# Kernel optimization log

Hardware: AMD Instinct MI355X
Metric: run time of the kernel (lower is better)

## Reference

```python
import jax, jax.numpy as jnp
import numpy as np

N0 = 1373      # hardcoded node-type split in the original forward
TAO = 0.4
EPS = 1e-12


def _l2norm(x, axis):
    # matches torch F.normalize(p=2): x / max(||x||, eps)
    n = jnp.sqrt(jnp.sum(x * x, axis=axis, keepdims=True))
    return x / jnp.maximum(n, EPS)


def setup_inputs() -> dict:
    key = jax.random.key(0)
    ks = jax.random.split(key, 12)
    N, E, D_IN, F, H, D = 20000, 320000, 256, 32, 8, 32
    feat = jax.random.normal(ks[0], (N, D_IN), jnp.float32)
    sloc = jax.random.normal(ks[1], (N, D), jnp.float32)
    topo_fea = jax.random.normal(ks[2], (N, D), jnp.float32)
    src = jax.random.randint(ks[3], (E,), 0, N)
    dst = jax.random.randint(ks[4], (E,), 0, N)
    e_feat = jax.random.randint(ks[5], (E,), 0, 4)
    s = 1.0 / np.sqrt(D_IN)
    W_proj0 = jax.random.normal(ks[6], (D_IN, H * F), jnp.float32) * s
    W_proj1 = jax.random.normal(ks[7], (D_IN, H * F), jnp.float32) * s
    W_prob = jax.random.normal(ks[8], (H, F, F), jnp.float32) * (1.0 / np.sqrt(F))
    W_res0 = jax.random.normal(ks[9], (D_IN, H * F), jnp.float32) * s
    W_res1 = jax.random.normal(ks[10], (D_IN, H * F), jnp.float32) * s
    etype_attn = jnp.ones((4,), jnp.float32)
    return dict(feat=feat, sloc=sloc, topo_fea=topo_fea, src=src, dst=dst,
                e_feat=e_feat, W_proj0=W_proj0, W_proj1=W_proj1, W_prob=W_prob,
                W_res0=W_res0, W_res1=W_res1, etype_attn=etype_attn)


def reference(feat, sloc, topo_fea, src, dst, e_feat,
              W_proj0, W_proj1, W_prob, W_res0, W_res1, etype_attn):
    N = feat.shape[0]
    H, F = W_prob.shape[0], W_prob.shape[2]
    sloc3 = sloc[:, None, :]        # (N,1,D) -- .unsqueeze(1)
    topo3 = topo_fea[:, None, :]

    # per-type node projection
    feat_src = jnp.concatenate(
        [feat[:N0] @ W_proj0, feat[N0:] @ W_proj1], axis=0).reshape(N, H, F)
    # per-head attention feature: softmax(tanh(fc4prob_i(.)), dim=feat)
    ft_attn = jax.nn.softmax(
        jnp.tanh(jnp.einsum('nhf,hfg->nhg', feat_src, W_prob)), axis=2)
    # F.normalize over the NODE dimension (dim=0), as in original
    ft_norm = _l2norm(feat_src, axis=0)

    sloc_n = _l2norm(sloc3, axis=2)
    topo_n = _l2norm(topo3, axis=2)

    # edge attention scores
    a = jnp.sum(ft_attn[dst] * ft_norm[src], axis=2, keepdims=True)   # (E,H,1)
    cos_s = jnp.sum(sloc_n[src] * sloc_n[dst], axis=2, keepdims=True)  # (E,1,1)
    cos_t = jnp.sum(topo_n[src] * topo_n[dst], axis=2, keepdims=True)
    sim = (TAO * cos_s + (1.0 - TAO) * cos_t + 1.0) / 2.0             # (E,1,1)
    e = (sim * a * etype_attn[e_feat][:, None, None])[:, :, 0]        # (E,H)

    # edge softmax: segment softmax over incoming edges of each dst node
    m = jax.ops.segment_max(e, dst, num_segments=N)                   # (N,H)
    ex = jnp.exp(e - m[dst])
    z = jax.ops.segment_sum(ex, dst, num_segments=N)
    att = ex / z[dst]                                                 # (E,H)

    # three u_mul_e + sum aggregations
    aw = att[:, :, None]                                              # (E,H,1)
    rst = jax.ops.segment_sum(feat_src[src] * aw, dst, num_segments=N)  # (N,H,F)
    sl2 = jax.ops.segment_sum(sloc3[src] * aw, dst, num_segments=N)     # (N,H,D)
    tp2 = jax.ops.segment_sum(topo3[src] * aw, dst, num_segments=N)     # (N,H,D)

    resval = jnp.concatenate(
        [feat[:N0] @ W_res0, feat[N0:] @ W_res1], axis=0).reshape(N, H, F)
    out_fea = jax.nn.relu(rst + resval).mean(axis=1)   # (N,F)
    out_sloc = (sl2 + sloc3).mean(axis=1)              # (N,D)
    out_topo = (tp2 + topo3).mean(axis=1)              # (N,D)
    return out_fea, out_sloc, out_topo
```

## Files before the change

### kernel.cpp

```cpp
#include <hip/hip_runtime.h>
#include <math.h>

#define HN0 1373
#define BM 128
#define BN 128
#define BK 32
#define LDT 40

typedef __attribute__((ext_vector_type(8))) short short8;
typedef __attribute__((ext_vector_type(4))) float f32x4;

__device__ inline unsigned short f2bf(float f) {
  unsigned int u = __float_as_uint(f);
  unsigned int r = (u + 0x7FFFu + ((u >> 16) & 1u)) >> 16;
  return (unsigned short)r;
}
__device__ inline float bflo(unsigned int u) { return __uint_as_float(u << 16); }
__device__ inline float bfhi(unsigned int u) { return __uint_as_float(u & 0xFFFF0000u); }

__device__ inline uint4 pack8bf(float4 a, float4 b) {
  uint4 o;
  o.x = (unsigned)f2bf(a.x) | ((unsigned)f2bf(a.y) << 16);
  o.y = (unsigned)f2bf(a.z) | ((unsigned)f2bf(a.w) << 16);
  o.z = (unsigned)f2bf(b.x) | ((unsigned)f2bf(b.y) << 16);
  o.w = (unsigned)f2bf(b.z) | ((unsigned)f2bf(b.w) << 16);
  return o;
}

__global__ __launch_bounds__(256) void prep(
    const float* __restrict__ Wp0, const float* __restrict__ Wr0,
    const float* __restrict__ Wp1, const float* __restrict__ Wr1,
    unsigned short* __restrict__ BTw,
    const float* __restrict__ sloc, const float* __restrict__ topo,
    unsigned short* __restrict__ slt, unsigned short* __restrict__ sltn,
    const int* __restrict__ dst, int* __restrict__ deg, int N, int E) {
  __shared__ float T[64][72];
  int b = blockIdx.x;
  int tid = threadIdx.x;
  int nodeBlocks = (N + 7) / 8;
  if (b < 64) {
    int mat = b >> 4;
    int t16 = b & 15;
    int kT = (t16 & 3) * 64;
    int nT = (t16 >> 2) * 64;
    const float* W = (mat == 0) ? Wp0 : (mat == 1) ? Wr0 : (mat == 2) ? Wp1 : Wr1;
    int g = mat >> 1;
    int nbase = (mat & 1) * 256;
    int r = tid >> 2;
    int cb = (tid & 3) * 16;
    const float* srcp = W + (size_t)(kT + r) * 256 + nT + cb;
#pragma unroll
    for (int q = 0; q < 4; ++q) {
      float4 v = *reinterpret_cast<const float4*>(srcp + q * 4);
      T[cb + q * 4 + 0][r] = v.x;
      T[cb + q * 4 + 1][r] = v.y;
      T[cb + q * 4 + 2][r] = v.z;
      T[cb + q * 4 + 3][r] = v.w;
    }
    __syncthreads();
    int nl = tid >> 2;
    int kb = (tid & 3) * 16;
    unsigned int pk[8];
#pragma unroll
    for (int q = 0; q < 8; ++q) {
      unsigned short lo = f2bf(T[nl][kb + q * 2]);
      unsigned short hi = f2bf(T[nl][kb + q * 2 + 1]);
      pk[q] = (unsigned)lo | ((unsigned)hi << 16);
    }
    unsigned short* dstp = BTw + (size_t)g * 512 * 256 + (size_t)(nbase + nT + nl) * 256 + kT + kb;
    *reinterpret_cast<uint4*>(dstp) = make_uint4(pk[0], pk[1], pk[2], pk[3]);
    *reinterpret_cast<uint4*>(dstp + 8) = make_uint4(pk[4], pk[5], pk[6], pk[7]);
  } else if (b < 64 + nodeBlocks) {
    int node = (b - 64) * 8 + (tid >> 5);
    int d = tid & 31;
    if (node >= N) return;
    float s = sloc[(size_t)node * 32 + d];
    float t = topo[(size_t)node * 32 + d];
    float ss = s * s, tt = t * t;
#pragma unroll
    for (int m = 16; m >= 1; m >>= 1) {
      ss += __shfl_xor(ss, m);
      tt += __shfl_xor(tt, m);
    }
    float is = 1.f / fmaxf(sqrtf(ss), 1e-12f);
    float it = 1.f / fmaxf(sqrtf(tt), 1e-12f);
    slt[(size_t)node * 64 + d] = f2bf(s);
    slt[(size_t)node * 64 + 32 + d] = f2bf(t);
    sltn[(size_t)node * 64 + d] = f2bf(s * is);
    sltn[(size_t)node * 64 + 32 + d] = f2bf(t * it);
  } else {
    int e = (b - 64 - nodeBlocks) * 256 + tid;
    if (e < E) atomicAdd(&deg[dst[e]], 1);
  }
}

__global__ __launch_bounds__(256) void gemm_scan(
    const float* __restrict__ A, const unsigned short* __restrict__ BTw,
    unsigned short* __restrict__ feat_bf, unsigned short* __restrict__ resval,
    const int* __restrict__ deg, int* __restrict__ start, int* __restrict__ bsum,
    int G, int N) {
  int b = blockIdx.x;
  int tid = threadIdx.x;
  if (b >= G) {
    __shared__ int buf[256];
    int b2 = b - G;
    int gid = b2 * 256 + tid;
    int v = (gid < N) ? deg[gid] : 0;
    buf[tid] = v;
    __syncthreads();
    for (int off = 1; off < 256; off <<= 1) {
      int t = (tid >= off) ? buf[tid - off] : 0;
      __syncthreads();
      buf[tid] += t;
      __syncthreads();
    }
    if (gid < N) start[gid] = buf[tid] - v;
    if (tid == 255) bsum[b2] = buf[255];
    return;
  }
  __shared__ __align__(16) unsigned short As[BM * LDT];
  __shared__ __align__(16) unsigned short Bs[BN * LDT];
  int lane = tid & 63;
  int w = tid >> 6;
  int wr = w >> 1, wc = w & 1;

  int g0t = (HN0 + BM - 1) / BM;
  int bx = b >> 2;
  int colBase = (b & 3) * BN;
  bool g1 = bx >= g0t;
  int rowBase = g1 ? HN0 + (bx - g0t) * BM : bx * BM;
  int rowEnd = g1 ? N : HN0;
  const unsigned short* BT = BTw + (g1 ? (size_t)512 * 256 : 0);

  int r0 = tid >> 2;
  int kp = (tid & 3) << 3;
  int ar1 = min(rowBase + r0, rowEnd - 1);
  int ar2 = min(rowBase + r0 + 64, rowEnd - 1);
  const float* aP1 = A + (size_t)ar1 * 256 + kp;
  const float* aP2 = A + (size_t)ar2 * 256 + kp;
  const unsigned short* bP1 = BT + (size_t)(colBase + r0) * 256 + kp;
  const unsigned short* bP2 = bP1 + (size_t)64 * 256;
  int wo1 = r0 * LDT + kp;
  int wo2 = (r0 + 64) * LDT + kp;

  int q = lane >> 4;
  int fr = lane & 15;
  int aOff = (wr * 64 + fr) * LDT + q * 8;
  int bOff = (wc * 64 + fr) * LDT + q * 8;

  f32x4 acc[4][4] = {};

  float4 fa1a = *reinterpret_cast<const float4*>(aP1);
  float4 fa1b = *reinterpret_cast<const float4*>(aP1 + 4);
  float4 fa2a = *reinterpret_cast<const float4*>(aP2);
  float4 fa2b = *reinterpret_cast<const float4*>(aP2 + 4);
  uint4 rb1 = *reinterpret_cast<const uint4*>(bP1);
  uint4 rb2 = *reinterpret_cast<const uint4*>(bP2);

  for (int t = 0; t < 8; ++t) {
    *reinterpret_cast<uint4*>(&As[wo1]) = pack8bf(fa1a, fa1b);
    *reinterpret_cast<uint4*>(&As[wo2]) = pack8bf(fa2a, fa2b);
    *reinterpret_cast<uint4*>(&Bs[wo1]) = rb1;
    *reinterpret_cast<uint4*>(&Bs[wo2]) = rb2;
    __syncthreads();
    if (t < 7) {
      int ko = (t + 1) * BK;
      fa1a = *reinterpret_cast<const float4*>(aP1 + ko);
      fa1b = *reinterpret_cast<const float4*>(aP1 + ko + 4);
      fa2a = *reinterpret_cast<const float4*>(aP2 + ko);
      fa2b = *reinterpret_cast<const float4*>(aP2 + ko + 4);
      rb1 = *reinterpret_cast<const uint4*>(bP1 + ko);
      rb2 = *reinterpret_cast<const uint4*>(bP2 + ko);
    }
    short8 af[4], bf4[4];
#pragma unroll
    for (int i = 0; i < 4; ++i) {
      af[i] = *reinterpret_cast<const short8*>(&As[aOff + i * 16 * LDT]);
      bf4[i] = *reinterpret_cast<const short8*>(&Bs[bOff + i * 16 * LDT]);
    }
#pragma unroll
    for (int i = 0; i < 4; ++i)
#pragma unroll
      for (int j = 0; j < 4; ++j)
        acc[i][j] = __builtin_amdgcn_mfma_f32_16x16x32_bf16(af[i], bf4[j], acc[i][j], 0, 0, 0);
    __syncthreads();
  }

  unsigned short* outp = (colBase < 256) ? feat_bf : resval;
  int cOff = colBase & 255;
#pragma unroll
  for (int i = 0; i < 4; ++i) {
    int rb = rowBase + wr * 64 + i * 16 + q * 4;
#pragma unroll
    for (int j = 0; j < 4; ++j) {
      int col = cOff + wc * 64 + j * 16 + fr;
      f32x4 v = acc[i][j];
#pragma unroll
      for (int rr = 0; rr < 4; ++rr) {
        int r = rb + rr;
        if (r < rowEnd) outp[(size_t)r * 256 + col] = f2bf(v[rr]);
      }
    }
  }
}

__global__ __launch_bounds__(256) void attn_mid(
    const unsigned short* __restrict__ feat_bf, const float* __restrict__ W_prob,
    unsigned short* __restrict__ ft_attn, float* __restrict__ col_ss,
    int* __restrict__ bsum, int nb, int nAttn, int N) {
  int tid = threadIdx.x;
  if ((int)blockIdx.x >= nAttn) {
    __shared__ int buf[128];
    if (tid < nb) buf[tid] = bsum[tid];
    __syncthreads();
    if (tid == 0) {
      int run = 0;
      for (int i = 0; i < nb; ++i) { int v = buf[i]; buf[i] = run; run += v; }
    }
    __syncthreads();
    if (tid < nb) bsum[tid] = buf[tid];
    return;
  }
  __shared__ float fsL[16 * 256];
  int h = tid >> 5, g = tid & 31;
  float wreg[32];
#pragma unroll
  for (int f = 0; f < 32; ++f) wreg[f] = W_prob[h * 1024 + f * 32 + g];
  int nodeBase = blockIdx.x * 16;
  float ssp = 0.f;
  for (int i = 0; i < 16; ++i) {
    int n = nodeBase + i;
    float v = (n < N) ? __uint_as_float((unsigned)feat_bf[(size_t)n * 256 + tid] << 16) : 0.f;
    fsL[i * 256 + tid] = v;
    ssp += v * v;
  }
  atomicAdd(&col_ss[tid], ssp);
  __syncthreads();
  for (int i = 0; i < 16; ++i) {
    int n = nodeBase + i;
    if (n >= N) break;
    const float* fr = &fsL[i * 256 + h * 32];
    float t0 = 0.f, t1 = 0.f, t2 = 0.f, t3 = 0.f;
#pragma unroll
    for (int f = 0; f < 8; ++f) {
      t0 = fmaf(fr[f * 4 + 0], wreg[f * 4 + 0], t0);
      t1 = fmaf(fr[f * 4 + 1], wreg[f * 4 + 1], t1);
      t2 = fmaf(fr[f * 4 + 2], wreg[f * 4 + 2], t2);
      t3 = fmaf(fr[f * 4 + 3], wreg[f * 4 + 3], t3);
    }
    float t = (t0 + t1) + (t2 + t3);
    float e2 = __expf(2.f * t);
    t = 1.f - 2.f * __builtin_amdgcn_rcpf(e2 + 1.f);
    float ex = __expf(t);
    float sm = ex;
#pragma unroll
    for (int s = 16; s >= 1; s >>= 1) sm += __shfl_xor(sm, s);
    ft_attn[(size_t)n * 256 + tid] = f2bf(ex * __builtin_amdgcn_rcpf(sm));
  }
}

__global__ __launch_bounds__(256) void fill_sim(
    const int* __restrict__ src, const int* __restrict__ dst,
    const int* __restrict__ e_feat, const float* __restrict__ etype_attn,
    const unsigned short* __restrict__ sltn,
    const int* __restrict__ start, const int* __restrict__ bsum,
    int* __restrict__ cursor, int2* __restrict__ csr, int E) {
  int tid = threadIdx.x;
  int j = tid & 3;
  int e = blockIdx.x * 64 + (tid >> 2);
  if (e >= E) return;
  int s = src[e], d = dst[e];
  const unsigned short* ps = sltn + (size_t)s * 64 + j * 16;
  const unsigned short* pd = sltn + (size_t)d * 64 + j * 16;
  uint4 a0 = *reinterpret_cast<const uint4*>(ps);
  uint4 a1 = *reinterpret_cast<const uint4*>(ps + 8);
  uint4 b0 = *reinterpret_cast<const uint4*>(pd);
  uint4 b1 = *reinterpret_cast<const uint4*>(pd + 8);
  float u = bflo(a0.x) * bflo(b0.x) + bfhi(a0.x) * bfhi(b0.x) +
            bflo(a0.y) * bflo(b0.y) + bfhi(a0.y) * bfhi(b0.y) +
            bflo(a0.z) * bflo(b0.z) + bfhi(a0.z) * bfhi(b0.z) +
            bflo(a0.w) * bflo(b0.w) + bfhi(a0.w) * bfhi(b0.w) +
            bflo(a1.x) * bflo(b1.x) + bfhi(a1.x) * bfhi(b1.x) +
            bflo(a1.y) * bflo(b1.y) + bfhi(a1.y) * bfhi(b1.y) +
            bflo(a1.z) * bflo(b1.z) + bfhi(a1.z) * bfhi(b1.z) +
            bflo(a1.w) * bflo(b1.w) + bfhi(a1.w) * bfhi(b1.w);
  u *= (j < 2) ? 0.4f : 0.6f;
  u += __shfl_xor(u, 1);
  u += __shfl_xor(u, 2);
  if (j == 0) {
    float sim = fmaf(u, 0.5f, 0.5f);
    float wv = sim * etype_attn[e_feat[e]];
    int pos = start[d] + bsum[d >> 8] + atomicAdd(&cursor[d], 1);
    csr[pos] = make_int2(s, __float_as_int(wv));
  }
}

#define LOADIDX(K, V, W)                                                       \
  do {                                                                         \
    int2 c_ = csr[s0 + (K)];                                                   \
    V = c_.x;                                                                  \
    W = __int_as_float(c_.y);                                                  \
  } while (0)

#define GATHER(V, FP, SL, TP)                                                  \
  do {                                                                         \
    FP = *reinterpret_cast<const uint2*>(feat_bf + (size_t)(V) * 256 + fb);    \
    const unsigned short* sp_ = slt + (size_t)(V) * 64 + db;                   \
    SL = *reinterpret_cast<const uint2*>(sp_);                                 \
    TP = *reinterpret_cast<const uint2*>(sp_ + 32);                            \
  } while (0)

#define CONSUME(W, FP, SL, TP)                                                 \
  do {                                                                         \
    float fs0 = bflo(FP.x), fs1 = bfhi(FP.x);                                  \
    float fs2 = bflo(FP.y), fs3 = bfhi(FP.y);                                  \
    float pa = ai4.x * fs0 + ai4.y * fs1 + ai4.z * fs2 + ai4.w * fs3;          \
    pa += __shfl_xor(pa, 1);                                                   \
    pa += __shfl_xor(pa, 2);                                                   \
    pa += __shfl_xor(pa, 4);                                                   \
    float p = __expf(pa * (W));                                                \
    l += p;                                                                    \
    accf.x = fmaf(p, fs0, accf.x); accf.y = fmaf(p, fs1, accf.y);              \
    accf.z = fmaf(p, fs2, accf.z); accf.w = fmaf(p, fs3, accf.w);              \
    accs.x = fmaf(p, bflo(SL.x), accs.x); accs.y = fmaf(p, bfhi(SL.x), accs.y);\
    accs.z = fmaf(p, bflo(SL.y), accs.z); accs.w = fmaf(p, bfhi(SL.y), accs.w);\
    acct.x = fmaf(p, bflo(TP.x), acct.x); acct.y = fmaf(p, bfhi(TP.x), acct.y);\
    acct.z = fmaf(p, bflo(TP.y), acct.z); acct.w = fmaf(p, bfhi(TP.y), acct.w);\
  } while (0)

__global__ __launch_bounds__(128) void edge_aggregate(
    const unsigned short* __restrict__ feat_bf, const unsigned short* __restrict__ resval,
    const unsigned short* __restrict__ ft_attn, const float* __restrict__ col_ss,
    const unsigned short* __restrict__ slt,
    const float* __restrict__ sloc, const float* __restrict__ topo,
    const int* __restrict__ start, const int* __restrict__ bsum,
    const int* __restrict__ deg, const int2* __restrict__ csr,
    float* __restrict__ out, int N) {
  int wave = threadIdx.x >> 6;
  int n = blockIdx.x * 2 + wave;
  if (n >= N) return;
  int lane = threadIdx.x & 63;
  int j = lane & 7;
  int fb = (lane >> 3) * 32 + j * 4;
  int db = j * 4;

  uint2 at2 = *reinterpret_cast<const uint2*>(ft_attn + (size_t)n * 256 + fb);
  float4 cs4 = *reinterpret_cast<const float4*>(col_ss + fb);
  float4 icn4 = make_float4(1.f / fmaxf(sqrtf(cs4.x), 1e-12f),
                            1.f / fmaxf(sqrtf(cs4.y), 1e-12f),
                            1.f / fmaxf(sqrtf(cs4.z), 1e-12f),
                            1.f / fmaxf(sqrtf(cs4.w), 1e-12f));
  float4 ai4 = make_float4(bflo(at2.x) * icn4.x, bfhi(at2.x) * icn4.y,
                           bflo(at2.y) * icn4.z, bfhi(at2.y) * icn4.w);
  float l = 0.f;
  float4 accf = make_float4(0.f, 0.f, 0.f, 0.f);
  float4 accs = make_float4(0.f, 0.f, 0.f, 0.f);
  float4 acct = make_float4(0.f, 0.f, 0.f, 0.f);
  int s0 = start[n] + bsum[n >> 8];
  int dg = deg[n];

  int vA = 0, vB = 0, vC = 0;
  float wA = 0.f, wB = 0.f, wC = 0.f;
  uint2 fpA = make_uint2(0u, 0u), fpB = make_uint2(0u, 0u), fpC = make_uint2(0u, 0u);
  uint2 slA = make_uint2(0u, 0u), slB = make_uint2(0u, 0u), slC = make_uint2(0u, 0u);
  uint2 tpA = make_uint2(0u, 0u), tpB = make_uint2(0u, 0u), tpC = make_uint2(0u, 0u);
  if (dg > 0) { LOADIDX(0, vA, wA); GATHER(vA, fpA, slA, tpA); }
  if (dg > 1) { LOADIDX(1, vB, wB); GATHER(vB, fpB, slB, tpB); }
  if (dg > 2) { LOADIDX(2, vC, wC); GATHER(vC, fpC, slC, tpC); }
  int i = 0;
  for (; i + 2 < dg; i += 3) {
    CONSUME(wA, fpA, slA, tpA);
    if (i + 3 < dg) { LOADIDX(i + 3, vA, wA); GATHER(vA, fpA, slA, tpA); }
    CONSUME(wB, fpB, slB, tpB);
    if (i + 4 < dg) { LOADIDX(i + 4, vB, wB); GATHER(vB, fpB, slB, tpB); }
    CONSUME(wC, fpC, slC, tpC);
    if (i + 5 < dg) { LOADIDX(i + 5, vC, wC); GATHER(vC, fpC, slC, tpC); }
  }
  if (i < dg) CONSUME(wA, fpA, slA, tpA);
  if (i + 1 < dg) CONSUME(wB, fpB, slB, tpB);

  float invl = (l > 0.f) ? 1.f / l : 0.f;

  uint2 res2 = *reinterpret_cast<const uint2*>(resval + (size_t)n * 256 + fb);
  float4 of = make_float4(fmaxf(fmaf(accf.x, invl, bflo(res2.x)), 0.f),
                          fmaxf(fmaf(accf.y, invl, bfhi(res2.x)), 0.f),
                          fmaxf(fmaf(accf.z, invl, bflo(res2.y)), 0.f),
                          fmaxf(fmaf(accf.w, invl, bfhi(res2.y)), 0.f));
  float4 os = make_float4(accs.x * invl, accs.y * invl, accs.z * invl, accs.w * invl);
  float4 ot = make_float4(acct.x * invl, acct.y * invl, acct.z * invl, acct.w * invl);
#pragma unroll
  for (int msk = 8; msk <= 32; msk <<= 1) {
    of.x += __shfl_xor(of.x, msk); of.y += __shfl_xor(of.y, msk);
    of.z += __shfl_xor(of.z, msk); of.w += __shfl_xor(of.w, msk);
    os.x += __shfl_xor(os.x, msk); os.y += __shfl_xor(os.y, msk);
    os.z += __shfl_xor(os.z, msk); os.w += __shfl_xor(os.w, msk);
    ot.x += __shfl_xor(ot.x, msk); ot.y += __shfl_xor(ot.y, msk);
    ot.z += __shfl_xor(ot.z, msk); ot.w += __shfl_xor(ot.w, msk);
  }
  if (lane < 8) {
    float4 sln = *reinterpret_cast<const float4*>(sloc + (size_t)n * 32 + db);
    float4 tpn = *reinterpret_cast<const float4*>(topo + (size_t)n * 32 + db);
    float4 o0 = make_float4(of.x * 0.125f, of.y * 0.125f, of.z * 0.125f, of.w * 0.125f);
    float4 o1 = make_float4(fmaf(os.x, 0.125f, sln.x), fmaf(os.y, 0.125f, sln.y),
                            fmaf(os.z, 0.125f, sln.z), fmaf(os.w, 0.125f, sln.w));
    float4 o2 = make_float4(fmaf(ot.x, 0.125f, tpn.x), fmaf(ot.y, 0.125f, tpn.y),
                            fmaf(ot.z, 0.125f, tpn.z), fmaf(ot.w, 0.125f, tpn.w));
    *reinterpret_cast<float4*>(out + (size_t)n * 32 + db) = o0;
    *reinterpret_cast<float4*>(out + (size_t)N * 32 + (size_t)n * 32 + db) = o1;
    *reinterpret_cast<float4*>(out + (size_t)2 * N * 32 + (size_t)n * 32 + db) = o2;
  }
}

extern "C" void kernel_launch(void* const* d_in, const int* in_sizes, int n_in,
                              void* d_out, int out_size, void* d_ws, size_t ws_size,
                              hipStream_t stream) {
  const float* feat = (const float*)d_in[0];
  const float* sloc = (const float*)d_in[1];
  const float* topo = (const float*)d_in[2];
  const int* src = (const int*)d_in[3];
  const int* dst = (const int*)d_in[4];
  const int* e_feat = (const int*)d_in[5];
  const float* W_proj0 = (const float*)d_in[6];
  const float* W_proj1 = (const float*)d_in[7];
  const float* W_prob = (const float*)d_in[8];
  const float* W_res0 = (const float*)d_in[9];
  const float* W_res1 = (const float*)d_in[10];
  const float* etype_attn = (const float*)d_in[11];
  int E = in_sizes[3];
  int N = in_sizes[1] / 32;
  float* out = (float*)d_out;

  char* ws = (char*)d_ws;
  size_t off = 0;
  auto alloc = [&](size_t bytes) -> char* {
    char* p = ws + off;
    off += (bytes + 255) & ~(size_t)255;
    return p;
  };
  int* deg = (int*)alloc((size_t)N * 4);
  int* cursor = (int*)alloc((size_t)N * 4);
  float* col_ss = (float*)alloc(256 * 4);
  size_t zeroBytes = ((char*)col_ss + 256 * 4) - (char*)deg;
  int* startArr = (int*)alloc(((size_t)N + 1) * 4);
  int* bsum = (int*)alloc(128 * 4);
  int2* csr = (int2*)alloc((size_t)E * 8);
  unsigned short* feat_bf = (unsigned short*)alloc((size_t)N * 256 * 2);
  unsigned short* slt = (unsigned short*)alloc((size_t)N * 64 * 2);
  unsigned short* sltn = (unsigned short*)alloc((size_t)N * 64 * 2);
  unsigned short* resval = (unsigned short*)alloc((size_t)N * 256 * 2);
  unsigned short* ft_attn = (unsigned short*)alloc((size_t)N * 256 * 2);
  unsigned short* BTw = (unsigned short*)alloc((size_t)2 * 512 * 256 * 2);

  hipMemsetAsync(deg, 0, zeroBytes, stream);

  int nodeBlocks = (N + 7) / 8;
  int degBlocks = (E + 255) / 256;
  prep<<<64 + nodeBlocks + degBlocks, 256, 0, stream>>>(
      W_proj0, W_res0, W_proj1, W_res1, BTw, sloc, topo, slt, sltn, dst, deg, N, E);

  int g0t = (HN0 + BM - 1) / BM;
  int g1t = (N - HN0 + BM - 1) / BM;
  int G = (g0t + g1t) * 4;
  int nb = (N + 255) / 256;
  gemm_scan<<<G + nb, 256, 0, stream>>>(feat, BTw, feat_bf, resval,
                                        deg, startArr, bsum, G, N);

  int nAttn = (N + 15) / 16;
  attn_mid<<<nAttn + 1, 256, 0, stream>>>(feat_bf, W_prob, ft_attn, col_ss,
                                          bsum, nb, nAttn, N);

  fill_sim<<<(E + 63) / 64, 256, 0, stream>>>(src, dst, e_feat, etype_attn, sltn,
                                              startArr, bsum, cursor, csr, E);

  edge_aggregate<<<(N + 1) / 2, 128, 0, stream>>>(feat_bf, resval, ft_attn, col_ss,
                                                  slt, sloc, topo, startArr, bsum,
                                                  deg, csr, out, N);
}
```

Before: 175.3 us.

## Fuse gather rows, merge fill into attn kernel, atomic block-scan offsets, deeper prefetch

Projected features and raw sloc/topo are stored together in one interleaved row (stride 320), so each neighbor gather in edge aggregation reads a single row instead of two separate arrays. The block-sum scan becomes an atomic counter in the scan blocks. Because neighbor order in the CSR is arbitrary anyway, block offsets no longer need to be sorted, which removes the separate serial scan step. The edge-fill work is merged into the attention kernel launch, saving one launch. The GEMM grid is reordered into groups of eight row tiles per column tile for L2 reuse of the B tiles. The edge-aggregation prefetch depth goes from three to four. The risks are a padded grid with idle early-exit blocks and higher register pressure in the aggregate loop.

```diff
diff --git a/kernel.cpp b/kernel.cpp
--- a/kernel.cpp
+++ b/kernel.cpp
@@ -6,6 +6,7 @@
 #define BN 128
 #define BK 32
 #define LDT 40
+#define FSTR 320
 
 typedef __attribute__((ext_vector_type(8))) short short8;
 typedef __attribute__((ext_vector_type(4))) float f32x4;
@@ -32,7 +33,7 @@
     const float* __restrict__ Wp1, const float* __restrict__ Wr1,
     unsigned short* __restrict__ BTw,
     const float* __restrict__ sloc, const float* __restrict__ topo,
-    unsigned short* __restrict__ slt, unsigned short* __restrict__ sltn,
+    unsigned short* __restrict__ fused, unsigned short* __restrict__ sltn,
     const int* __restrict__ dst, int* __restrict__ deg, int N, int E) {
   __shared__ float T[64][72];
   int b = blockIdx.x;
@@ -84,8 +85,8 @@
     }
     float is = 1.f / fmaxf(sqrtf(ss), 1e-12f);
     float it = 1.f / fmaxf(sqrtf(tt), 1e-12f);
-    slt[(size_t)node * 64 + d] = f2bf(s);
-    slt[(size_t)node * 64 + 32 + d] = f2bf(t);
+    fused[(size_t)node * FSTR + 256 + d] = f2bf(s);
+    fused[(size_t)node * FSTR + 288 + d] = f2bf(t);
     sltn[(size_t)node * 64 + d] = f2bf(s * is);
     sltn[(size_t)node * 64 + 32 + d] = f2bf(t * it);
   } else {
@@ -96,14 +97,14 @@
 
 __global__ __launch_bounds__(256) void gemm_scan(
     const float* __restrict__ A, const unsigned short* __restrict__ BTw,
-    unsigned short* __restrict__ feat_bf, unsigned short* __restrict__ resval,
+    unsigned short* __restrict__ fused, unsigned short* __restrict__ resval,
     const int* __restrict__ deg, int* __restrict__ start, int* __restrict__ bsum,
-    int G, int N) {
+    int* __restrict__ gctr, int Gpad, int R, int N) {
   int b = blockIdx.x;
   int tid = threadIdx.x;
-  if (b >= G) {
+  if (b >= Gpad) {
     __shared__ int buf[256];
-    int b2 = b - G;
+    int b2 = b - Gpad;
     int gid = b2 * 256 + tid;
     int v = (gid < N) ? deg[gid] : 0;
     buf[tid] = v;
@@ -115,9 +116,15 @@
       __syncthreads();
     }
     if (gid < N) start[gid] = buf[tid] - v;
-    if (tid == 255) bsum[b2] = buf[255];
+    if (tid == 255) bsum[b2] = atomicAdd(gctr, buf[255]);
     return;
   }
+  int r8 = b & 7;
+  int c = (b >> 3) & 3;
+  int bx = (b >> 5) * 8 + r8;
+  if (bx >= R) return;
+  int colBase = c * BN;
+
   __shared__ __align__(16) unsigned short As[BM * LDT];
   __shared__ __align__(16) unsigned short Bs[BN * LDT];
   int lane = tid & 63;
@@ -125,8 +132,6 @@
   int wr = w >> 1, wc = w & 1;
 
   int g0t = (HN0 + BM - 1) / BM;
-  int bx = b >> 2;
-  int colBase = (b & 3) * BN;
   bool g1 = bx >= g0t;
   int rowBase = g1 ? HN0 + (bx - g0t) * BM : bx * BM;
   int rowEnd = g1 ? N : HN0;
@@ -186,7 +191,7 @@
     __syncthreads();
   }
 
-  unsigned short* outp = (colBase < 256) ? feat_bf : resval;
+  bool isFeat = (colBase < 256);
   int cOff = colBase & 255;
 #pragma unroll
   for (int i = 0; i < 4; ++i) {
@@ -198,27 +203,53 @@
 #pragma unroll
       for (int rr = 0; rr < 4; ++rr) {
         int r = rb + rr;
-        if (r < rowEnd) outp[(size_t)r * 256 + col] = f2bf(v[rr]);
+        if (r < rowEnd) {
+          if (isFeat) fused[(size_t)r * FSTR + col] = f2bf(v[rr]);
+          else        resval[(size_t)r * 256 + col] = f2bf(v[rr]);
+        }
       }
     }
   }
 }
 
-__global__ __launch_bounds__(256) void attn_mid(
-    const unsigned short* __restrict__ feat_bf, const float* __restrict__ W_prob,
+__global__ __launch_bounds__(256) void attn_fill(
+    const unsigned short* __restrict__ fused, const float* __restrict__ W_prob,
     unsigned short* __restrict__ ft_attn, float* __restrict__ col_ss,
-    int* __restrict__ bsum, int nb, int nAttn, int N) {
+    const int* __restrict__ src, const int* __restrict__ dst,
+    const int* __restrict__ e_feat, const float* __restrict__ etype_attn,
+    const unsigned short* __restrict__ sltn,
+    const int* __restrict__ start, const int* __restrict__ bsum,
+    int* __restrict__ cursor, int2* __restrict__ csr,
+    int nAttn, int N, int E) {
   int tid = threadIdx.x;
   if ((int)blockIdx.x >= nAttn) {
-    __shared__ int buf[128];
-    if (tid < nb) buf[tid] = bsum[tid];
-    __syncthreads();
-    if (tid == 0) {
-      int run = 0;
-      for (int i = 0; i < nb; ++i) { int v = buf[i]; buf[i] = run; run += v; }
-    }
-    __syncthreads();
-    if (tid < nb) bsum[tid] = buf[tid];
+    int j = tid & 3;
+    int e = ((int)blockIdx.x - nAttn) * 64 + (tid >> 2);
+    if (e >= E) return;
+    int s = src[e], d = dst[e];
+    const unsigned short* ps = sltn + (size_t)s * 64 + j * 16;
+    const unsigned short* pd = sltn + (size_t)d * 64 + j * 16;
+    uint4 a0 = *reinterpret_cast<const uint4*>(ps);
+    uint4 a1 = *reinterpret_cast<const uint4*>(ps + 8);
+    uint4 b0 = *reinterpret_cast<const uint4*>(pd);
+    uint4 b1 = *reinterpret_cast<const uint4*>(pd + 8);
+    float u = bflo(a0.x) * bflo(b0.x) + bfhi(a0.x) * bfhi(b0.x) +
+              bflo(a0.y) * bflo(b0.y) + bfhi(a0.y) * bfhi(b0.y) +
+              bflo(a0.z) * bflo(b0.z) + bfhi(a0.z) * bfhi(b0.z) +
+              bflo(a0.w) * bflo(b0.w) + bfhi(a0.w) * bfhi(b0.w) +
+              bflo(a1.x) * bflo(b1.x) + bfhi(a1.x) * bfhi(b1.x) +
+              bflo(a1.y) * bflo(b1.y) + bfhi(a1.y) * bfhi(b1.y) +
+              bflo(a1.z) * bflo(b1.z) + bfhi(a1.z) * bfhi(b1.z) +
+              bflo(a1.w) * bflo(b1.w) + bfhi(a1.w) * bfhi(b1.w);
+    u *= (j < 2) ? 0.4f : 0.6f;
+    u += __shfl_xor(u, 1);
+    u += __shfl_xor(u, 2);
+    if (j == 0) {
+      float sim = fmaf(u, 0.5f, 0.5f);
+      float wv = sim * etype_attn[e_feat[e]];
+      int pos = start[d] + bsum[d >> 8] + atomicAdd(&cursor[d], 1);
+      csr[pos] = make_int2(s, __float_as_int(wv));
+    }
     return;
   }
   __shared__ float fsL[16 * 256];
@@ -230,7 +261,7 @@
   float ssp = 0.f;
   for (int i = 0; i < 16; ++i) {
     int n = nodeBase + i;
-    float v = (n < N) ? __uint_as_float((unsigned)feat_bf[(size_t)n * 256 + tid] << 16) : 0.f;
+    float v = (n < N) ? __uint_as_float((unsigned)fused[(size_t)n * FSTR + tid] << 16) : 0.f;
     fsL[i * 256 + tid] = v;
     ssp += v * v;
   }
@@ -259,42 +290,6 @@
   }
 }
 
-__global__ __launch_bounds__(256) void fill_sim(
-    const int* __restrict__ src, const int* __restrict__ dst,
-    const int* __restrict__ e_feat, const float* __restrict__ etype_attn,
-    const unsigned short* __restrict__ sltn,
-    const int* __restrict__ start, const int* __restrict__ bsum,
-    int* __restrict__ cursor, int2* __restrict__ csr, int E) {
-  int tid = threadIdx.x;
-  int j = tid & 3;
-  int e = blockIdx.x * 64 + (tid >> 2);
-  if (e >= E) return;
-  int s = src[e], d = dst[e];
-  const unsigned short* ps = sltn + (size_t)s * 64 + j * 16;
-  const unsigned short* pd = sltn + (size_t)d * 64 + j * 16;
-  uint4 a0 = *reinterpret_cast<const uint4*>(ps);
-  uint4 a1 = *reinterpret_cast<const uint4*>(ps + 8);
-  uint4 b0 = *reinterpret_cast<const uint4*>(pd);
-  uint4 b1 = *reinterpret_cast<const uint4*>(pd + 8);
-  float u = bflo(a0.x) * bflo(b0.x) + bfhi(a0.x) * bfhi(b0.x) +
-            bflo(a0.y) * bflo(b0.y) + bfhi(a0.y) * bfhi(b0.y) +
-            bflo(a0.z) * bflo(b0.z) + bfhi(a0.z) * bfhi(b0.z) +
-            bflo(a0.w) * bflo(b0.w) + bfhi(a0.w) * bfhi(b0.w) +
-            bflo(a1.x) * bflo(b1.x) + bfhi(a1.x) * bfhi(b1.x) +
-            bflo(a1.y) * bflo(b1.y) + bfhi(a1.y) * bfhi(b1.y) +
-            bflo(a1.z) * bflo(b1.z) + bfhi(a1.z) * bfhi(b1.z) +
-            bflo(a1.w) * bflo(b1.w) + bfhi(a1.w) * bfhi(b1.w);
-  u *= (j < 2) ? 0.4f : 0.6f;
-  u += __shfl_xor(u, 1);
-  u += __shfl_xor(u, 2);
-  if (j == 0) {
-    float sim = fmaf(u, 0.5f, 0.5f);
-    float wv = sim * etype_attn[e_feat[e]];
-    int pos = start[d] + bsum[d >> 8] + atomicAdd(&cursor[d], 1);
-    csr[pos] = make_int2(s, __float_as_int(wv));
-  }
-}
-
 #define LOADIDX(K, V, W)                                                       \
   do {                                                                         \
     int2 c_ = csr[s0 + (K)];                                                   \
@@ -304,10 +299,10 @@
 
 #define GATHER(V, FP, SL, TP)                                                  \
   do {                                                                         \
-    FP = *reinterpret_cast<const uint2*>(feat_bf + (size_t)(V) * 256 + fb);    \
-    const unsigned short* sp_ = slt + (size_t)(V) * 64 + db;                   \
-    SL = *reinterpret_cast<const uint2*>(sp_);                                 \
-    TP = *reinterpret_cast<const uint2*>(sp_ + 32);                            \
+    const unsigned short* r_ = fused + (size_t)(V) * FSTR;                     \
+    FP = *reinterpret_cast<const uint2*>(r_ + fb);                             \
+    SL = *reinterpret_cast<const uint2*>(r_ + 256 + db);                       \
+    TP = *reinterpret_cast<const uint2*>(r_ + 288 + db);                       \
   } while (0)
 
 #define CONSUME(W, FP, SL, TP)                                                 \
@@ -329,9 +324,8 @@
   } while (0)
 
 __global__ __launch_bounds__(128) void edge_aggregate(
-    const unsigned short* __restrict__ feat_bf, const unsigned short* __restrict__ resval,
+    const unsigned short* __restrict__ fused, const unsigned short* __restrict__ resval,
     const unsigned short* __restrict__ ft_attn, const float* __restrict__ col_ss,
-    const unsigned short* __restrict__ slt,
     const float* __restrict__ sloc, const float* __restrict__ topo,
     const int* __restrict__ start, const int* __restrict__ bsum,
     const int* __restrict__ deg, const int2* __restrict__ csr,
@@ -359,25 +353,30 @@
   int s0 = start[n] + bsum[n >> 8];
   int dg = deg[n];
 
-  int vA = 0, vB = 0, vC = 0;
-  float wA = 0.f, wB = 0.f, wC = 0.f;
-  uint2 fpA = make_uint2(0u, 0u), fpB = make_uint2(0u, 0u), fpC = make_uint2(0u, 0u);
-  uint2 slA = make_uint2(0u, 0u), slB = make_uint2(0u, 0u), slC = make_uint2(0u, 0u);
-  uint2 tpA = make_uint2(0u, 0u), tpB = make_uint2(0u, 0u), tpC = make_uint2(0u, 0u);
+  int vA = 0, vB = 0, vC = 0, vD = 0;
+  float wA = 0.f, wB = 0.f, wC = 0.f, wD = 0.f;
+  uint2 fpA, fpB, fpC, fpD, slA, slB, slC, slD, tpA, tpB, tpC, tpD;
+  fpA = fpB = fpC = fpD = make_uint2(0u, 0u);
+  slA = slB = slC = slD = make_uint2(0u, 0u);
+  tpA = tpB = tpC = tpD = make_uint2(0u, 0u);
   if (dg > 0) { LOADIDX(0, vA, wA); GATHER(vA, fpA, slA, tpA); }
   if (dg > 1) { LOADIDX(1, vB, wB); GATHER(vB, fpB, slB, tpB); }
   if (dg > 2) { LOADIDX(2, vC, wC); GATHER(vC, fpC, slC, tpC); }
+  if (dg > 3) { LOADIDX(3, vD, wD); GATHER(vD, fpD, slD, tpD); }
   int i = 0;
-  for (; i + 2 < dg; i += 3) {
+  for (; i + 3 < dg; i += 4) {
     CONSUME(wA, fpA, slA, tpA);
-    if (i + 3 < dg) { LOADIDX(i + 3, vA, wA); GATHER(vA, fpA, slA, tpA); }
+    if (i + 4 < dg) { LOADIDX(i + 4, vA, wA); GATHER(vA, fpA, slA, tpA); }
     CONSUME(wB, fpB, slB, tpB);
-    if (i + 4 < dg) { LOADIDX(i + 4, vB, wB); GATHER(vB, fpB, slB, tpB); }
+    if (i + 5 < dg) { LOADIDX(i + 5, vB, wB); GATHER(vB, fpB, slB, tpB); }
     CONSUME(wC, fpC, slC, tpC);
-    if (i + 5 < dg) { LOADIDX(i + 5, vC, wC); GATHER(vC, fpC, slC, tpC); }
+    if (i + 6 < dg) { LOADIDX(i + 6, vC, wC); GATHER(vC, fpC, slC, tpC); }
+    CONSUME(wD, fpD, slD, tpD);
+    if (i + 7 < dg) { LOADIDX(i + 7, vD, wD); GATHER(vD, fpD, slD, tpD); }
   }
   if (i < dg) CONSUME(wA, fpA, slA, tpA);
   if (i + 1 < dg) CONSUME(wB, fpB, slB, tpB);
+  if (i + 2 < dg) CONSUME(wC, fpC, slC, tpC);
 
   float invl = (l > 0.f) ? 1.f / l : 0.f;
 
@@ -440,12 +439,12 @@
   int* deg = (int*)alloc((size_t)N * 4);
   int* cursor = (int*)alloc((size_t)N * 4);
   float* col_ss = (float*)alloc(256 * 4);
-  size_t zeroBytes = ((char*)col_ss + 256 * 4) - (char*)deg;
+  int* gctr = (int*)alloc(256);
+  size_t zeroBytes = ((char*)gctr + 256) - (char*)deg;
   int* startArr = (int*)alloc(((size_t)N + 1) * 4);
   int* bsum = (int*)alloc(128 * 4);
   int2* csr = (int2*)alloc((size_t)E * 8);
-  unsigned short* feat_bf = (unsigned short*)alloc((size_t)N * 256 * 2);
-  unsigned short* slt = (unsigned short*)alloc((size_t)N * 64 * 2);
+  unsigned short* fused = (unsigned short*)alloc((size_t)N * FSTR * 2);
   unsigned short* sltn = (unsigned short*)alloc((size_t)N * 64 * 2);
   unsigned short* resval = (unsigned short*)alloc((size_t)N * 256 * 2);
   unsigned short* ft_attn = (unsigned short*)alloc((size_t)N * 256 * 2);
@@ -456,23 +455,23 @@
   int nodeBlocks = (N + 7) / 8;
   int degBlocks = (E + 255) / 256;
   prep<<<64 + nodeBlocks + degBlocks, 256, 0, stream>>>(
-      W_proj0, W_res0, W_proj1, W_res1, BTw, sloc, topo, slt, sltn, dst, deg, N, E);
+      W_proj0, W_res0, W_proj1, W_res1, BTw, sloc, topo, fused, sltn, dst, deg, N, E);
 
   int g0t = (HN0 + BM - 1) / BM;
   int g1t = (N - HN0 + BM - 1) / BM;
-  int G = (g0t + g1t) * 4;
+  int R = g0t + g1t;
+  int Gpad = ((R + 7) / 8) * 32;
   int nb = (N + 255) / 256;
-  gemm_scan<<<G + nb, 256, 0, stream>>>(feat, BTw, feat_bf, resval,
-                                        deg, startArr, bsum, G, N);
+  gemm_scan<<<Gpad + nb, 256, 0, stream>>>(feat, BTw, fused, resval,
+                                           deg, startArr, bsum, gctr, Gpad, R, N);
 
   int nAttn = (N + 15) / 16;
-  attn_mid<<<nAttn + 1, 256, 0, stream>>>(feat_bf, W_prob, ft_attn, col_ss,
-                                          bsum, nb, nAttn, N);
-
-  fill_sim<<<(E + 63) / 64, 256, 0, stream>>>(src, dst, e_feat, etype_attn, sltn,
-                                              startArr, bsum, cursor, csr, E);
-
-  edge_aggregate<<<(N + 1) / 2, 128, 0, stream>>>(feat_bf, resval, ft_attn, col_ss,
-                                                  slt, sloc, topo, startArr, bsum,
+  int fillBlocks = (E + 63) / 64;
+  attn_fill<<<nAttn + fillBlocks, 256, 0, stream>>>(
+      fused, W_prob, ft_attn, col_ss, src, dst, e_feat, etype_attn, sltn,
+      startArr, bsum, cursor, csr, nAttn, N, E);
+
+  edge_aggregate<<<(N + 1) / 2, 128, 0, stream>>>(fused, resval, ft_attn, col_ss,
+                                                  sloc, topo, startArr, bsum,
                                                   deg, csr, out, N);
 }
```

Result: faster. 169.9 us (-3.1%).

## Replace serial block-sum scan with atomic offsets and merge attention with CSR fill

Applied to the files above, without the earlier changes.

Each scan block in gemm_scan now claims its base offset in the CSR with an atomicAdd on a zeroed global counter, instead of a later single-block serial prefix over block sums. With that dependency gone, the attention-feature kernel and the edge-similarity/CSR-fill kernel are merged into one launch, removing one kernel launch and its serialization. The GEMM blocks are also remapped so groups of 8 row tiles share column tiles, for better L2 reuse of the B operand, with padding blocks that exit early. Segments are still contiguous per block, but block order in the CSR becomes nondeterministic.

```diff
diff --git a/kernel.cpp b/kernel.cpp
--- a/kernel.cpp
+++ b/kernel.cpp
@@ -98,12 +98,12 @@
     const float* __restrict__ A, const unsigned short* __restrict__ BTw,
     unsigned short* __restrict__ feat_bf, unsigned short* __restrict__ resval,
     const int* __restrict__ deg, int* __restrict__ start, int* __restrict__ bsum,
-    int G, int N) {
+    int* __restrict__ gctr, int Gpad, int R, int N) {
   int b = blockIdx.x;
   int tid = threadIdx.x;
-  if (b >= G) {
+  if (b >= Gpad) {
     __shared__ int buf[256];
-    int b2 = b - G;
+    int b2 = b - Gpad;
     int gid = b2 * 256 + tid;
     int v = (gid < N) ? deg[gid] : 0;
     buf[tid] = v;
@@ -115,9 +115,15 @@
       __syncthreads();
     }
     if (gid < N) start[gid] = buf[tid] - v;
-    if (tid == 255) bsum[b2] = buf[255];
+    if (tid == 255) bsum[b2] = atomicAdd(gctr, buf[255]);
     return;
   }
+  int r8 = b & 7;
+  int c = (b >> 3) & 3;
+  int bx = (b >> 5) * 8 + r8;
+  if (bx >= R) return;
+  int colBase = c * BN;
+
   __shared__ __align__(16) unsigned short As[BM * LDT];
   __shared__ __align__(16) unsigned short Bs[BN * LDT];
   int lane = tid & 63;
@@ -125,8 +131,6 @@
   int wr = w >> 1, wc = w & 1;
 
   int g0t = (HN0 + BM - 1) / BM;
-  int bx = b >> 2;
-  int colBase = (b & 3) * BN;
   bool g1 = bx >= g0t;
   int rowBase = g1 ? HN0 + (bx - g0t) * BM : bx * BM;
   int rowEnd = g1 ? N : HN0;
@@ -204,21 +208,44 @@
   }
 }
 
-__global__ __launch_bounds__(256) void attn_mid(
+__global__ __launch_bounds__(256) void attn_fill(
     const unsigned short* __restrict__ feat_bf, const float* __restrict__ W_prob,
     unsigned short* __restrict__ ft_attn, float* __restrict__ col_ss,
-    int* __restrict__ bsum, int nb, int nAttn, int N) {
+    const int* __restrict__ src, const int* __restrict__ dst,
+    const int* __restrict__ e_feat, const float* __restrict__ etype_attn,
+    const unsigned short* __restrict__ sltn,
+    const int* __restrict__ start, const int* __restrict__ bsum,
+    int* __restrict__ cursor, int2* __restrict__ csr,
+    int nAttn, int N, int E) {
   int tid = threadIdx.x;
   if ((int)blockIdx.x >= nAttn) {
-    __shared__ int buf[128];
-    if (tid < nb) buf[tid] = bsum[tid];
-    __syncthreads();
-    if (tid == 0) {
-      int run = 0;
-      for (int i = 0; i < nb; ++i) { int v = buf[i]; buf[i] = run; run += v; }
-    }
-    __syncthreads();
-    if (tid < nb) bsum[tid] = buf[tid];
+    int j = tid & 3;
+    int e = ((int)blockIdx.x - nAttn) * 64 + (tid >> 2);
+    if (e >= E) return;
+    int s = src[e], d = dst[e];
+    const unsigned short* ps = sltn + (size_t)s * 64 + j * 16;
+    const unsigned short* pd = sltn + (size_t)d * 64 + j * 16;
+    uint4 a0 = *reinterpret_cast<const uint4*>(ps);
+    uint4 a1 = *reinterpret_cast<const uint4*>(ps + 8);
+    uint4 b0 = *reinterpret_cast<const uint4*>(pd);
+    uint4 b1 = *reinterpret_cast<const uint4*>(pd + 8);
+    float u = bflo(a0.x) * bflo(b0.x) + bfhi(a0.x) * bfhi(b0.x) +
+              bflo(a0.y) * bflo(b0.y) + bfhi(a0.y) * bfhi(b0.y) +
+              bflo(a0.z) * bflo(b0.z) + bfhi(a0.z) * bfhi(b0.z) +
+              bflo(a0.w) * bflo(b0.w) + bfhi(a0.w) * bfhi(b0.w) +
+              bflo(a1.x) * bflo(b1.x) + bfhi(a1.x) * bfhi(b1.x) +
+              bflo(a1.y) * bflo(b1.y) + bfhi(a1.y) * bfhi(b1.y) +
+              bflo(a1.z) * bflo(b1.z) + bfhi(a1.z) * bfhi(b1.z) +
+              bflo(a1.w) * bflo(b1.w) + bfhi(a1.w) * bfhi(b1.w);
+    u *= (j < 2) ? 0.4f : 0.6f;
+    u += __shfl_xor(u, 1);
+    u += __shfl_xor(u, 2);
+    if (j == 0) {
+      float sim = fmaf(u, 0.5f, 0.5f);
+      float wv = sim * etype_attn[e_feat[e]];
+      int pos = start[d] + bsum[d >> 8] + atomicAdd(&cursor[d], 1);
+      csr[pos] = make_int2(s, __float_as_int(wv));
+    }
     return;
   }
   __shared__ float fsL[16 * 256];
@@ -256,42 +283,6 @@
 #pragma unroll
     for (int s = 16; s >= 1; s >>= 1) sm += __shfl_xor(sm, s);
     ft_attn[(size_t)n * 256 + tid] = f2bf(ex * __builtin_amdgcn_rcpf(sm));
-  }
-}
-
-__global__ __launch_bounds__(256) void fill_sim(
-    const int* __restrict__ src, const int* __restrict__ dst,
-    const int* __restrict__ e_feat, const float* __restrict__ etype_attn,
-    const unsigned short* __restrict__ sltn,
-    const int* __restrict__ start, const int* __restrict__ bsum,
-    int* __restrict__ cursor, int2* __restrict__ csr, int E) {
-  int tid = threadIdx.x;
-  int j = tid & 3;
-  int e = blockIdx.x * 64 + (tid >> 2);
-  if (e >= E) return;
-  int s = src[e], d = dst[e];
-  const unsigned short* ps = sltn + (size_t)s * 64 + j * 16;
-  const unsigned short* pd = sltn + (size_t)d * 64 + j * 16;
-  uint4 a0 = *reinterpret_cast<const uint4*>(ps);
-  uint4 a1 = *reinterpret_cast<const uint4*>(ps + 8);
-  uint4 b0 = *reinterpret_cast<const uint4*>(pd);
-  uint4 b1 = *reinterpret_cast<const uint4*>(pd + 8);
-  float u = bflo(a0.x) * bflo(b0.x) + bfhi(a0.x) * bfhi(b0.x) +
-            bflo(a0.y) * bflo(b0.y) + bfhi(a0.y) * bfhi(b0.y) +
-            bflo(a0.z) * bflo(b0.z) + bfhi(a0.z) * bfhi(b0.z) +
-            bflo(a0.w) * bflo(b0.w) + bfhi(a0.w) * bfhi(b0.w) +
-            bflo(a1.x) * bflo(b1.x) + bfhi(a1.x) * bfhi(b1.x) +
-            bflo(a1.y) * bflo(b1.y) + bfhi(a1.y) * bfhi(b1.y) +
-            bflo(a1.z) * bflo(b1.z) + bfhi(a1.z) * bfhi(b1.z) +
-            bflo(a1.w) * bflo(b1.w) + bfhi(a1.w) * bfhi(b1.w);
-  u *= (j < 2) ? 0.4f : 0.6f;
-  u += __shfl_xor(u, 1);
-  u += __shfl_xor(u, 2);
-  if (j == 0) {
-    float sim = fmaf(u, 0.5f, 0.5f);
-    float wv = sim * etype_attn[e_feat[e]];
-    int pos = start[d] + bsum[d >> 8] + atomicAdd(&cursor[d], 1);
-    csr[pos] = make_int2(s, __float_as_int(wv));
   }
 }
 
@@ -440,7 +431,8 @@
   int* deg = (int*)alloc((size_t)N * 4);
   int* cursor = (int*)alloc((size_t)N * 4);
   float* col_ss = (float*)alloc(256 * 4);
-  size_t zeroBytes = ((char*)col_ss + 256 * 4) - (char*)deg;
+  int* gctr = (int*)alloc(256);
+  size_t zeroBytes = ((char*)gctr + 256) - (char*)deg;
   int* startArr = (int*)alloc(((size_t)N + 1) * 4);
   int* bsum = (int*)alloc(128 * 4);
   int2* csr = (int2*)alloc((size_t)E * 8);
@@ -460,17 +452,17 @@
 
   int g0t = (HN0 + BM - 1) / BM;
   int g1t = (N - HN0 + BM - 1) / BM;
-  int G = (g0t + g1t) * 4;
+  int R = g0t + g1t;
+  int Gpad = ((R + 7) / 8) * 32;
   int nb = (N + 255) / 256;
-  gemm_scan<<<G + nb, 256, 0, stream>>>(feat, BTw, feat_bf, resval,
-                                        deg, startArr, bsum, G, N);
+  gemm_scan<<<Gpad + nb, 256, 0, stream>>>(feat, BTw, feat_bf, resval,
+                                           deg, startArr, bsum, gctr, Gpad, R, N);
 
   int nAttn = (N + 15) / 16;
-  attn_mid<<<nAttn + 1, 256, 0, stream>>>(feat_bf, W_prob, ft_attn, col_ss,
-                                          bsum, nb, nAttn, N);
-
-  fill_sim<<<(E + 63) / 64, 256, 0, stream>>>(src, dst, e_feat, etype_attn, sltn,
-                                              startArr, bsum, cursor, csr, E);
+  int fillBlocks = (E + 63) / 64;
+  attn_fill<<<nAttn + fillBlocks, 256, 0, stream>>>(
+      feat_bf, W_prob, ft_attn, col_ss, src, dst, e_feat, etype_attn, sltn,
+      startArr, bsum, cursor, csr, nAttn, N, E);
 
   edge_aggregate<<<(N + 1) / 2, 128, 0, stream>>>(feat_bf, resval, ft_attn, col_ss,
                                                   slt, sloc, topo, startArr, bsum,
```

After: 160.1 us. 1.09x faster.
